# Performance work log

Measured on AMD Instinct MI355X. Metric: run time of the kernel, lower is better.

Reference implementation:

```python
import jax, jax.numpy as jnp
import numpy as np

S, H, A = 16384, 1024, 1024


def setup_inputs() -> dict:
    key = jax.random.key(0)
    k1, k2, k3, k4, k5, k6 = jax.random.split(key, 6)
    enc_out = jax.random.normal(k1, (S, 1, H), dtype=jnp.float32)
    dec_h = jax.random.normal(k2, (1, H), dtype=jnp.float32)
    mask = jax.random.randint(k3, (S, 1), 0, 2) == 1  # bool [S,1]
    # learned params (torch Linear stores weight as [out, in]; y = x @ W.T)
    W2_dec = jax.random.normal(k4, (A, H), dtype=jnp.float32) * 0.02
    W1_enc = jax.random.normal(k5, (A, H), dtype=jnp.float32) * 0.02
    V = jax.random.normal(k6, (1, A), dtype=jnp.float32) * 0.02
    return {"enc_out": enc_out, "dec_h": dec_h, "mask": mask,
            "W2_dec": W2_dec, "W1_enc": W1_enc, "V": V}


def reference(enc_out, dec_h, mask, W2_dec, W1_enc, V):
    enc = jnp.squeeze(enc_out, axis=1)            # [S, H]
    d = dec_h @ W2_dec.T                          # [1, A]
    e = enc @ W1_enc.T                            # [S, A]
    u = jnp.tanh(d + e) @ V.T                     # [S, 1]
    u = jnp.where(mask, -jnp.inf, u)              # masked logits (returned, like in-place fill)
    a = jax.nn.softmax(u, axis=0)                 # softmax over seq dim
    out = jnp.sum(a * enc, axis=0)                # [H]
    return (out, u)
```

## Files before the change

### kernel.cpp

```cpp
#include <hip/hip_runtime.h>
#include <math.h>
#include <stdint.h>

#define S_DIM 16384
#define H_DIM 1024
#define A_DIM 1024

#define MASK_NEG (-3.0e38f)

typedef __attribute__((ext_vector_type(8))) _Float16 f16x8;
typedef __attribute__((ext_vector_type(4))) float f32x4;
typedef __attribute__((address_space(3))) uint32_t as3_u32;
typedef __attribute__((address_space(1))) uint32_t as1_u32;

__device__ __forceinline__ float fast_tanh(float x) {
    float e = __expf(2.0f * x);
    return 1.0f - 2.0f * __builtin_amdgcn_rcpf(e + 1.0f);
}


__global__ __launch_bounds__(256) void prep_kernel(
        const float* __restrict__ enc, _Float16* __restrict__ enc_h,
        const float* __restrict__ W1, _Float16* __restrict__ W1_h,
        const float* __restrict__ dec_h, const float* __restrict__ W2,
        float* __restrict__ d, float* __restrict__ u_acc,
        const void* __restrict__ mask, int* __restrict__ mflag) {
    const int b = blockIdx.x;
    const int t = threadIdx.x;
    if (b < 1088) {
        const int cb = b;
        const float* src;
        _Float16* dst;
        int tb, kt;
        if (cb < 1024) { src = enc;  dst = enc_h; tb = cb >> 4; kt = cb & 15; }
        else           { src = W1;   dst = W1_h;  tb = (cb - 1024) >> 4; kt = (cb - 1024) & 15; }
        uint4* dchunk = (uint4*)dst + (size_t)(tb * 16 + kt) * 1024;
        const float* srow = src + (size_t)tb * 256 * H_DIM + kt * 32;
        #pragma unroll
        for (int it = 0; it < 4; ++it) {
            const int idx  = it * 256 + t;
            const int r    = idx >> 2;
            const int slot = idx & 3;
            const int cg   = (slot + (r >> 1)) & 3;
            const float* sp = srow + (size_t)r * H_DIM + cg * 8;
            float4 v0 = ((const float4*)sp)[0];
            float4 v1 = ((const float4*)sp)[1];
            union { _Float16 h[8]; uint4 u; } pk;
            pk.h[0] = (_Float16)v0.x; pk.h[1] = (_Float16)v0.y;
            pk.h[2] = (_Float16)v0.z; pk.h[3] = (_Float16)v0.w;
            pk.h[4] = (_Float16)v1.x; pk.h[5] = (_Float16)v1.y;
            pk.h[6] = (_Float16)v1.z; pk.h[7] = (_Float16)v1.w;
            dchunk[idx] = pk.u;
        }
        if (b < 64) u_acc[b * 256 + t] = 0.0f;
    } else if (b < 2112) {
        const int a = b - 1088;
        const float* row = W2 + (size_t)a * H_DIM;
        float s = 0.0f;
        for (int h = t; h < H_DIM; h += 256) s += dec_h[h] * row[h];
        #pragma unroll
        for (int off = 32; off; off >>= 1) s += __shfl_down(s, off, 64);
        __shared__ float wsum[4];
        if ((t & 63) == 0) wsum[t >> 6] = s;
        __syncthreads();
        if (t == 0) d[a] = wsum[0] + wsum[1] + wsum[2] + wsum[3];
    } else {
        const unsigned char* mb = (const unsigned char*)mask;
        unsigned int orv = 0;
        for (int i = t; i < S_DIM; i += 256)
            if (i & 3) orv |= mb[i];
        __shared__ int oflag;
        if (t == 0) oflag = 0;
        __syncthreads();
        if (orv) oflag = 1;
        __syncthreads();
        if (t == 0) mflag[0] = oflag;
    }
}

__global__ __launch_bounds__(512, 1) void fused_gemm_f16_2ph(
        const _Float16* __restrict__ Ag,
        const _Float16* __restrict__ Bg,
        const float* __restrict__ V,
        const float* __restrict__ d,
        float* __restrict__ u_acc) {
    __shared__ __align__(16) _Float16 AB[2][32768];

    const int tid  = threadIdx.x;
    const int wave = tid >> 6;
    const int lane = tid & 63;
    const int quad = lane >> 4;
    const int l16  = lane & 15;
    const int wm   = wave >> 2;
    const int wn   = wave & 3;
    const int s0   = blockIdx.x * 256;
    const int a0   = blockIdx.y * 256;

    const int rowoff = (wave & 3) * 64;
    const _Float16* gtile = ((wave < 4)
            ? Ag + (size_t)blockIdx.x * (16 * 8192)
            : Bg + (size_t)blockIdx.y * (16 * 8192))
          + rowoff * 32 + lane * 8;
    _Float16* lbase0 = &AB[0][((wave < 4) ? 0 : 8192) + rowoff * 32];

    const int sw = ((quad - (l16 >> 1)) & 3) * 8;
    int aoff[8], boff[4];
    #pragma unroll
    for (int mi = 0; mi < 8; ++mi)
        aoff[mi] = (wm * 128 + mi * 16 + l16) * 32 + sw;
    #pragma unroll
    for (int ni = 0; ni < 4; ++ni)
        boff[ni] = 8192 + (wn * 64 + ni * 16 + l16) * 32 + sw;

    f32x4 acc[8][4];
    #pragma unroll
    for (int mi = 0; mi < 8; ++mi)
        #pragma unroll
        for (int ni = 0; ni < 4; ++ni)
            acc[mi][ni] = (f32x4){0.f, 0.f, 0.f, 0.f};

    const _Float16* hAB = &AB[0][0];

    #pragma unroll
    for (int s = 0; s < 2; ++s)
        #pragma unroll
        for (int j = 0; j < 4; ++j)
            __builtin_amdgcn_global_load_lds(
                (const as1_u32*)(const void*)(gtile + s * 8192 + j * 512),
                (as3_u32*)(void*)(lbase0 + s * 16384 + j * 512), 16, 0, 0);

    for (int ph = 0; ph < 16; ++ph) {
        const int b = ph & 1;
        if (ph < 15) {
            #pragma unroll
            for (int s = 0; s < 2; ++s)
                #pragma unroll
                for (int j = 0; j < 4; ++j)
                    __builtin_amdgcn_global_load_lds(
                        (const as1_u32*)(const void*)(gtile + ((ph + 1) * 2 + s) * 8192 + j * 512),
                        (as3_u32*)(void*)(lbase0 + (b ^ 1) * 32768 + s * 16384 + j * 512),
                        16, 0, 0);
            asm volatile("s_waitcnt vmcnt(8)" ::: "memory");
        } else {
            asm volatile("s_waitcnt vmcnt(0)" ::: "memory");
        }
        __builtin_amdgcn_sched_barrier(0);
        __builtin_amdgcn_s_barrier();
        __builtin_amdgcn_sched_barrier(0);

        __builtin_amdgcn_s_setprio(1);
        #pragma unroll
        for (int s = 0; s < 2; ++s) {
            const int base = b * 32768 + s * 16384;
            f16x8 bf[4];
            #pragma unroll
            for (int ni = 0; ni < 4; ++ni)
                bf[ni] = *(const f16x8*)&hAB[base + boff[ni]];
            #pragma unroll
            for (int mi = 0; mi < 8; ++mi) {
                f16x8 af = *(const f16x8*)&hAB[base + aoff[mi]];
                #pragma unroll
                for (int ni = 0; ni < 4; ++ni)
                    acc[mi][ni] = __builtin_amdgcn_mfma_f32_16x16x32_f16(af, bf[ni], acc[mi][ni], 0, 0, 0);
            }
        }
        __builtin_amdgcn_s_setprio(0);
        __builtin_amdgcn_sched_barrier(0);

        if (ph < 15) {
            __builtin_amdgcn_s_barrier();
            __builtin_amdgcn_sched_barrier(0);
        }
    }

    float* P = (float*)&AB[0][0];
    float vv[4], dd[4];
    #pragma unroll
    for (int ni = 0; ni < 4; ++ni) {
        int c = a0 + wn * 64 + ni * 16 + l16;
        vv[ni] = V[c];
        dd[ni] = d[c];
    }
    #pragma unroll
    for (int mi = 0; mi < 8; ++mi) {
        #pragma unroll
        for (int reg = 0; reg < 4; ++reg) {
            float s = 0.0f;
            #pragma unroll
            for (int ni = 0; ni < 4; ++ni)
                s += vv[ni] * fast_tanh(dd[ni] + acc[mi][ni][reg]);
            #pragma unroll
            for (int off = 1; off < 16; off <<= 1)
                s += __shfl_xor(s, off, 64);
            if (l16 == 0)
                P[(wm * 128 + mi * 16 + quad * 4 + reg) * 4 + wn] = s;
        }
    }
    __syncthreads();
    if (tid < 256)
        atomicAdd(u_acc + s0 + tid,
                  P[tid * 4 + 0] + P[tid * 4 + 1] + P[tid * 4 + 2] + P[tid * 4 + 3]);
}

__global__ __launch_bounds__(512, 2) void fused_gemm_f16(
        const _Float16* __restrict__ Ag, const _Float16* __restrict__ Bg,
        const float* __restrict__ V, const float* __restrict__ d,
        float* __restrict__ u_acc) {
    __shared__ __align__(16) _Float16 AB[2][16384];

    const int tid  = threadIdx.x;
    const int wave = tid >> 6;
    const int lane = tid & 63;
    const int quad = lane >> 4;
    const int l16  = lane & 15;
    const int wm   = wave >> 2;
    const int wn   = wave & 3;
    const int s0   = blockIdx.x * 256;
    const int a0   = blockIdx.y * 256;

    const int rowoff = (wave & 3) * 64;
    const _Float16* gtile = ((wave < 4)
            ? Ag + (size_t)blockIdx.x * (16 * 8192)
            : Bg + (size_t)blockIdx.y * (16 * 8192))
          + rowoff * 32 + lane * 8;
    _Float16* lbase0 = &AB[0][((wave < 4) ? 0 : 8192) + rowoff * 32];

    const int sw = ((quad - (l16 >> 1)) & 3) * 8;
    int aoff[8], boff[4];
    #pragma unroll
    for (int mi = 0; mi < 8; ++mi)
        aoff[mi] = (wm * 128 + mi * 16 + l16) * 32 + sw;
    #pragma unroll
    for (int ni = 0; ni < 4; ++ni)
        boff[ni] = 8192 + (wn * 64 + ni * 16 + l16) * 32 + sw;

    f32x4 acc[8][4];
    #pragma unroll
    for (int mi = 0; mi < 8; ++mi)
        #pragma unroll
        for (int ni = 0; ni < 4; ++ni)
            acc[mi][ni] = (f32x4){0.f, 0.f, 0.f, 0.f};

    #pragma unroll
    for (int j = 0; j < 4; ++j)
        __builtin_amdgcn_global_load_lds(
            (const as1_u32*)(const void*)(gtile + j * 512),
            (as3_u32*)(void*)(lbase0 + j * 512), 16, 0, 0);
    __syncthreads();

    for (int kt = 0; kt < H_DIM / 32; kt += 2) {
        {
            #pragma unroll
            for (int j = 0; j < 4; ++j)
                __builtin_amdgcn_global_load_lds(
                    (const as1_u32*)(const void*)(gtile + (kt + 1) * 8192 + j * 512),
                    (as3_u32*)(void*)(lbase0 + 16384 + j * 512), 16, 0, 0);
        }
        {
            f16x8 bf[4];
            #pragma unroll
            for (int ni = 0; ni < 4; ++ni) bf[ni] = *(const f16x8*)&AB[0][boff[ni]];
            #pragma unroll
            for (int mi = 0; mi < 8; ++mi) {
                f16x8 af = *(const f16x8*)&AB[0][aoff[mi]];
                #pragma unroll
                for (int ni = 0; ni < 4; ++ni)
                    acc[mi][ni] = __builtin_amdgcn_mfma_f32_16x16x32_f16(af, bf[ni], acc[mi][ni], 0, 0, 0);
            }
        }
        __syncthreads();
        if (kt + 2 < H_DIM / 32) {
            #pragma unroll
            for (int j = 0; j < 4; ++j)
                __builtin_amdgcn_global_load_lds(
                    (const as1_u32*)(const void*)(gtile + (kt + 2) * 8192 + j * 512),
                    (as3_u32*)(void*)(lbase0 + j * 512), 16, 0, 0);
        }
        {
            f16x8 bf[4];
            #pragma unroll
            for (int ni = 0; ni < 4; ++ni) bf[ni] = *(const f16x8*)&AB[1][boff[ni]];
            #pragma unroll
            for (int mi = 0; mi < 8; ++mi) {
                f16x8 af = *(const f16x8*)&AB[1][aoff[mi]];
                #pragma unroll
                for (int ni = 0; ni < 4; ++ni)
                    acc[mi][ni] = __builtin_amdgcn_mfma_f32_16x16x32_f16(af, bf[ni], acc[mi][ni], 0, 0, 0);
            }
        }
        __syncthreads();
    }

    float* P = (float*)&AB[0][0];
    float vv[4], dd[4];
    #pragma unroll
    for (int ni = 0; ni < 4; ++ni) {
        int c = a0 + wn * 64 + ni * 16 + l16;
        vv[ni] = V[c];
        dd[ni] = d[c];
    }
    #pragma unroll
    for (int mi = 0; mi < 8; ++mi) {
        #pragma unroll
        for (int reg = 0; reg < 4; ++reg) {
            float s = 0.0f;
            #pragma unroll
            for (int ni = 0; ni < 4; ++ni)
                s += vv[ni] * fast_tanh(dd[ni] + acc[mi][ni][reg]);
            #pragma unroll
            for (int off = 1; off < 16; off <<= 1)
                s += __shfl_xor(s, off, 64);
            if (l16 == 0)
                P[(wm * 128 + mi * 16 + quad * 4 + reg) * 4 + wn] = s;
        }
    }
    __syncthreads();
    if (tid < 256)
        atomicAdd(u_acc + s0 + tid,
                  P[tid * 4 + 0] + P[tid * 4 + 1] + P[tid * 4 + 2] + P[tid * 4 + 3]);
}

__global__ __launch_bounds__(256) void fused_gemm(const float* __restrict__ enc,
                                                  const float* __restrict__ W1,
                                                  const float* __restrict__ V,
                                                  const float* __restrict__ d,
                                                  float* __restrict__ u_acc) {
    __shared__ __align__(16) float As[16][128 + 4];
    __shared__ __align__(16) float Bs[16][128 + 4];
    const int tid = threadIdx.x;
    const int tx = tid & 15, ty = tid >> 4;
    const int s0 = blockIdx.y * 128, a0 = blockIdx.x * 128;
    const int lr = tid >> 2, lc = tid & 3;
    float acc[8][8] = {};
    for (int kt = 0; kt < H_DIM / 16; ++kt) {
        const int k0 = kt * 16;
        float4 av0 = *(const float4*)(enc + (size_t)(s0 + lr)      * H_DIM + k0 + 4 * lc);
        float4 av1 = *(const float4*)(enc + (size_t)(s0 + lr + 64) * H_DIM + k0 + 4 * lc);
        float4 bv0 = *(const float4*)(W1  + (size_t)(a0 + lr)      * H_DIM + k0 + 4 * lc);
        float4 bv1 = *(const float4*)(W1  + (size_t)(a0 + lr + 64) * H_DIM + k0 + 4 * lc);
        __syncthreads();
        As[4*lc+0][lr] = av0.x; As[4*lc+1][lr] = av0.y; As[4*lc+2][lr] = av0.z; As[4*lc+3][lr] = av0.w;
        As[4*lc+0][lr+64] = av1.x; As[4*lc+1][lr+64] = av1.y; As[4*lc+2][lr+64] = av1.z; As[4*lc+3][lr+64] = av1.w;
        Bs[4*lc+0][lr] = bv0.x; Bs[4*lc+1][lr] = bv0.y; Bs[4*lc+2][lr] = bv0.z; Bs[4*lc+3][lr] = bv0.w;
        Bs[4*lc+0][lr+64] = bv1.x; Bs[4*lc+1][lr+64] = bv1.y; Bs[4*lc+2][lr+64] = bv1.z; Bs[4*lc+3][lr+64] = bv1.w;
        __syncthreads();
        #pragma unroll
        for (int k = 0; k < 16; ++k) {
            float4 A0 = *(const float4*)&As[k][8 * ty];
            float4 A1 = *(const float4*)&As[k][8 * ty + 4];
            float4 B0 = *(const float4*)&Bs[k][8 * tx];
            float4 B1 = *(const float4*)&Bs[k][8 * tx + 4];
            float ar[8] = {A0.x, A0.y, A0.z, A0.w, A1.x, A1.y, A1.z, A1.w};
            float br[8] = {B0.x, B0.y, B0.z, B0.w, B1.x, B1.y, B1.z, B1.w};
            #pragma unroll
            for (int i = 0; i < 8; ++i)
                #pragma unroll
                for (int j = 0; j < 8; ++j)
                    acc[i][j] = fmaf(ar[i], br[j], acc[i][j]);
        }
    }
    float vv[8], dd[8];
    #pragma unroll
    for (int j = 0; j < 8; ++j) { int c = a0 + 8 * tx + j; vv[j] = V[c]; dd[j] = d[c]; }
    float pu[8];
    #pragma unroll
    for (int i = 0; i < 8; ++i) {
        float s = 0.0f;
        #pragma unroll
        for (int j = 0; j < 8; ++j) s += vv[j] * fast_tanh(dd[j] + acc[i][j]);
        pu[i] = s;
    }
    __syncthreads();
    float* Pf = &As[0][0];
    #pragma unroll
    for (int i = 0; i < 8; ++i) Pf[(8 * ty + i) * 16 + tx] = pu[i];
    __syncthreads();
    if (tid < 128) {
        float s = 0.0f;
        #pragma unroll
        for (int j = 0; j < 16; ++j) s += Pf[tid * 16 + j];
        atomicAdd(u_acc + s0 + tid, s);
    }
}

__global__ __launch_bounds__(1024) void softmax_kernel(const float* __restrict__ u_acc,
                                                       const void* __restrict__ mask,
                                                       float* __restrict__ u_out,
                                                       float* __restrict__ p) {
    const int t = threadIdx.x;
    const unsigned char* mb = (const unsigned char*)mask;
    const int* mi = (const int*)mask;

    unsigned int orv = 0;
    for (int i = t; i < S_DIM; i += 1024)
        if (i & 3) orv |= mb[i];
    __shared__ int sflag;
    if (t == 0) sflag = 0;
    __syncthreads();
    if (orv) sflag = 1;
    __syncthreads();
    const int bytemask = sflag;

    float v[16];
    float lmax = -INFINITY;
    #pragma unroll
    for (int i = 0; i < 16; ++i) {
        int r = t + i * 1024;
        int m = bytemask ? (int)mb[r] : mi[r];
        float val = m ? MASK_NEG : u_acc[r];
        u_out[r] = val;
        v[i] = val;
        lmax = fmaxf(lmax, val);
    }

    __shared__ float red[16];
    __shared__ float sm, sdenom;
    #pragma unroll
    for (int off = 32; off; off >>= 1) lmax = fmaxf(lmax, __shfl_down(lmax, off, 64));
    int wid = t >> 6, lane = t & 63;
    if (lane == 0) red[wid] = lmax;
    __syncthreads();
    if (t == 0) {
        float m2 = -INFINITY;
        for (int i = 0; i < 16; ++i) m2 = fmaxf(m2, red[i]);
        sm = m2;
    }
    __syncthreads();
    const float m = sm;

    float lsum = 0.0f;
    #pragma unroll
    for (int i = 0; i < 16; ++i) {
        v[i] = expf(v[i] - m);
        lsum += v[i];
    }
    #pragma unroll
    for (int off = 32; off; off >>= 1) lsum += __shfl_down(lsum, off, 64);
    if (lane == 0) red[wid] = lsum;
    __syncthreads();
    if (t == 0) {
        float s2 = 0.0f;
        for (int i = 0; i < 16; ++i) s2 += red[i];
        sdenom = s2;
    }
    __syncthreads();
    const float inv = 1.0f / sdenom;
    #pragma unroll
    for (int i = 0; i < 16; ++i) p[t + i * 1024] = v[i] * inv;
}

__global__ __launch_bounds__(256) void tail_part(
        const _Float16* __restrict__ enc_h,
        const float* __restrict__ u_acc,
        const void* __restrict__ mask,
        const int* __restrict__ mflag,
        float* __restrict__ u_out,
        float* __restrict__ part,
        float* __restrict__ pm,
        float* __restrict__ pd) {
    const int t = threadIdx.x;
    const int b = blockIdx.x;
    const int s0 = b * 32;
    __shared__ float wsh[32];

    if (t < 32) {
        const int s = s0 + t;
        int msk = mflag[0] ? (int)((const unsigned char*)mask)[s]
                           : ((const int*)mask)[s];
        float val = msk ? MASK_NEG : u_acc[s];
        u_out[s] = val;
        float m_b = val;
        #pragma unroll
        for (int off = 16; off; off >>= 1)
            m_b = fmaxf(m_b, __shfl_xor(m_b, off, 64));
        float w = msk ? 0.0f : expf(val - m_b);
        wsh[t] = w;
        float D = w;
        #pragma unroll
        for (int off = 16; off; off >>= 1)
            D += __shfl_xor(D, off, 64);
        if (t == 0) { pm[b] = m_b; pd[b] = D; }
    }
    __syncthreads();

    const int kt    = t >> 3;
    const int cg    = (t >> 1) & 3;
    const int inner = (t & 1) * 4;
    float4 acc = {0.f, 0.f, 0.f, 0.f};
    for (int i = 0; i < 32; ++i) {
        float w = wsh[i];
        if (w != 0.0f) {
            const int s  = s0 + i;
            const int r  = s & 255;
            const int tb = s >> 8;
            const int slot = (cg - (r >> 1)) & 3;
            size_t off = ((size_t)(tb * 16 + kt) << 13) + (r << 5) + slot * 8 + inner;
            union { _Float16 h[4]; uint2 u; } e;
            e.u = *(const uint2*)(enc_h + off);
            acc.x += w * (float)e.h[0];
            acc.y += w * (float)e.h[1];
            acc.z += w * (float)e.h[2];
            acc.w += w * (float)e.h[3];
        }
    }
    ((float4*)(part + (size_t)b * 1024))[t] = acc;
}

__global__ __launch_bounds__(256) void tail_reduce(
        const float* __restrict__ part, const float* __restrict__ pm,
        const float* __restrict__ pd, float* __restrict__ out) {
    __shared__ float scale[512];
    __shared__ float red[256];
    __shared__ float ginv;
    const int t = threadIdx.x;

    red[t] = fmaxf(pm[t], pm[t + 256]);
    __syncthreads();
    #pragma unroll
    for (int off = 128; off; off >>= 1) {
        if (t < off) red[t] = fmaxf(red[t], red[t + off]);
        __syncthreads();
    }
    const float gm = red[0];
    __syncthreads();

    float sc0 = expf(pm[t] - gm);
    float sc1 = expf(pm[t + 256] - gm);
    scale[t] = sc0; scale[t + 256] = sc1;
    red[t] = sc0 * pd[t] + sc1 * pd[t + 256];
    __syncthreads();
    #pragma unroll
    for (int off = 128; off; off >>= 1) {
        if (t < off) red[t] += red[t + off];
        __syncthreads();
    }
    if (t == 0) ginv = 1.0f / red[0];
    __syncthreads();

    const int col = blockIdx.x * 16 + (t & 15);
    const int seg = t >> 4;
    float s = 0.0f;
    for (int b2 = seg * 32; b2 < seg * 32 + 32; ++b2)
        s += scale[b2] * part[(size_t)b2 * 1024 + col];
    red[t] = s;
    __syncthreads();
    if (t < 16) {
        float r = 0.0f;
        #pragma unroll
        for (int k = 0; k < 16; ++k) r += red[k * 16 + t];
        out[col] = r * ginv;
    }
}

__global__ __launch_bounds__(256) void weighted_sum(const float* __restrict__ enc,
                                                    const float* __restrict__ p,
                                                    float* __restrict__ out) {
    const int t = threadIdx.x;
    const int s0 = blockIdx.x * 32;
    const float4* encv = (const float4*)enc;
    float4 acc = {0.0f, 0.0f, 0.0f, 0.0f};
    for (int s = s0; s < s0 + 32; ++s) {
        float ps = p[s];
        float4 e = encv[(size_t)s * 256 + t];
        acc.x += ps * e.x; acc.y += ps * e.y; acc.z += ps * e.z; acc.w += ps * e.w;
    }
    atomicAdd(out + 4 * t + 0, acc.x);
    atomicAdd(out + 4 * t + 1, acc.y);
    atomicAdd(out + 4 * t + 2, acc.z);
    atomicAdd(out + 4 * t + 3, acc.w);
}
__global__ void zero_kernel(float* __restrict__ u_acc, float* __restrict__ out) {
    int i = blockIdx.x * 256 + threadIdx.x;
    if (i < S_DIM) u_acc[i] = 0.0f;
    if (i < H_DIM) out[i]   = 0.0f;
}
__global__ __launch_bounds__(256) void dec_proj(const float* __restrict__ dec_h,
                                                const float* __restrict__ W2,
                                                float* __restrict__ d) {
    int a = blockIdx.x;
    int t = threadIdx.x;
    const float* row = W2 + (size_t)a * H_DIM;
    float s = 0.0f;
    for (int h = t; h < H_DIM; h += 256) s += dec_h[h] * row[h];
    #pragma unroll
    for (int off = 32; off; off >>= 1) s += __shfl_down(s, off, 64);
    __shared__ float wsum[4];
    if ((t & 63) == 0) wsum[t >> 6] = s;
    __syncthreads();
    if (t == 0) d[a] = wsum[0] + wsum[1] + wsum[2] + wsum[3];
}

extern "C" void kernel_launch(void* const* d_in, const int* in_sizes, int n_in,
                              void* d_out, int out_size, void* d_ws, size_t ws_size,
                              hipStream_t stream) {
    const float* enc   = (const float*)d_in[0];
    const float* dec_h = (const float*)d_in[1];
    const void*  mask  = d_in[2];
    const float* W2    = (const float*)d_in[3];
    const float* W1    = (const float*)d_in[4];
    const float* V     = (const float*)d_in[5];

    float* out   = (float*)d_out;
    float* u_out = (float*)d_out + H_DIM;

    float* ws    = (float*)d_ws;
    float* d     = ws;
    float* u_acc = ws + A_DIM;
    float* p     = ws + A_DIM + S_DIM;
    float* pm    = p;
    float* pd    = p + 512;
    int*   mflag = (int*)(p + 1024);
    float* part  = ws + A_DIM + 2 * S_DIM;
    size_t f_end = (size_t)(A_DIM + 2 * S_DIM + 512 * 1024);
    _Float16* enc_h = (_Float16*)(ws + f_end);
    _Float16* W1_h  = enc_h + (size_t)S_DIM * H_DIM;
    size_t need_bytes = f_end * 4
                      + (size_t)S_DIM * H_DIM * 2
                      + (size_t)A_DIM * H_DIM * 2;

    int dev = 0;
    hipGetDevice(&dev);
    int max_lds = 0;
    hipDeviceGetAttribute(&max_lds, hipDeviceAttributeMaxSharedMemoryPerBlock, dev);

    if (ws_size >= need_bytes) {
        prep_kernel<<<2113, 256, 0, stream>>>(enc, enc_h, W1, W1_h,
                                              dec_h, W2, d, u_acc, mask, mflag);
        if (max_lds >= 131072) {
            fused_gemm_f16_2ph<<<dim3(S_DIM / 256, A_DIM / 256), 512, 0, stream>>>(
                enc_h, W1_h, V, d, u_acc);
        } else {
            fused_gemm_f16<<<dim3(S_DIM / 256, A_DIM / 256), 512, 0, stream>>>(
                enc_h, W1_h, V, d, u_acc);
        }
        tail_part<<<S_DIM / 32, 256, 0, stream>>>(enc_h, u_acc, mask, mflag,
                                                  u_out, part, pm, pd);
        tail_reduce<<<64, 256, 0, stream>>>(part, pm, pd, out);
    } else {
        zero_kernel<<<64, 256, 0, stream>>>(u_acc, out);
        dec_proj<<<A_DIM, 256, 0, stream>>>(dec_h, W2, d);
        fused_gemm<<<dim3(A_DIM / 128, S_DIM / 128), 256, 0, stream>>>(enc, W1, V, d, u_acc);
        softmax_kernel<<<1, 1024, 0, stream>>>(u_acc, mask, u_out, p);
        weighted_sum<<<S_DIM / 32, 256, 0, stream>>>(enc, p, out);
    }
}
```

Before: 168.3 us.

## Fuse fp32-to-fp16 conversion of encoder into GEMM loader, drop enc_h staging

Removes the separate pass that converts the whole encoder matrix to a swizzled fp16 copy. The GEMM's A-side waves now load fp32 rows directly, convert them in registers and store them into LDS, with loads for the next stage issued around the compute halves. The tail kernel reads fp32 encoder rows directly instead of the fp16 copy. This saves a 64MB read plus 32MB write round trip. In exchange, A tiles are re-read in fp32 by each of the 4 A-column blocks, which doubles A-side traffic, and the register-staged loads may stall MFMA more than the async LDS loads did. The fallback fp16 GEMM variant is deleted.

```diff
diff --git a/kernel.cpp b/kernel.cpp
--- a/kernel.cpp
+++ b/kernel.cpp
@@ -20,22 +20,16 @@
 
 
 __global__ __launch_bounds__(256) void prep_kernel(
-        const float* __restrict__ enc, _Float16* __restrict__ enc_h,
         const float* __restrict__ W1, _Float16* __restrict__ W1_h,
         const float* __restrict__ dec_h, const float* __restrict__ W2,
         float* __restrict__ d, float* __restrict__ u_acc,
         const void* __restrict__ mask, int* __restrict__ mflag) {
     const int b = blockIdx.x;
     const int t = threadIdx.x;
-    if (b < 1088) {
-        const int cb = b;
-        const float* src;
-        _Float16* dst;
-        int tb, kt;
-        if (cb < 1024) { src = enc;  dst = enc_h; tb = cb >> 4; kt = cb & 15; }
-        else           { src = W1;   dst = W1_h;  tb = (cb - 1024) >> 4; kt = (cb - 1024) & 15; }
-        uint4* dchunk = (uint4*)dst + (size_t)(tb * 16 + kt) * 1024;
-        const float* srow = src + (size_t)tb * 256 * H_DIM + kt * 32;
+    if (b < 64) {
+        const int tb = b >> 4, kt = b & 15;
+        uint4* dchunk = (uint4*)W1_h + (size_t)(tb * 16 + kt) * 1024;
+        const float* srow = W1 + (size_t)tb * 256 * H_DIM + kt * 32;
         #pragma unroll
         for (int it = 0; it < 4; ++it) {
             const int idx  = it * 256 + t;
@@ -52,9 +46,9 @@
             pk.h[6] = (_Float16)v1.z; pk.h[7] = (_Float16)v1.w;
             dchunk[idx] = pk.u;
         }
-        if (b < 64) u_acc[b * 256 + t] = 0.0f;
-    } else if (b < 2112) {
-        const int a = b - 1088;
+        u_acc[b * 256 + t] = 0.0f;
+    } else if (b < 1088) {
+        const int a = b - 64;
         const float* row = W2 + (size_t)a * H_DIM;
         float s = 0.0f;
         for (int h = t; h < H_DIM; h += 256) s += dec_h[h] * row[h];
@@ -79,7 +73,7 @@
 }
 
 __global__ __launch_bounds__(512, 1) void fused_gemm_f16_2ph(
-        const _Float16* __restrict__ Ag,
+        const float* __restrict__ enc,
         const _Float16* __restrict__ Bg,
         const float* __restrict__ V,
         const float* __restrict__ d,
@@ -97,11 +91,16 @@
     const int a0   = blockIdx.y * 256;
 
     const int rowoff = (wave & 3) * 64;
-    const _Float16* gtile = ((wave < 4)
-            ? Ag + (size_t)blockIdx.x * (16 * 8192)
-            : Bg + (size_t)blockIdx.y * (16 * 8192))
-          + rowoff * 32 + lane * 8;
-    _Float16* lbase0 = &AB[0][((wave < 4) ? 0 : 8192) + rowoff * 32];
+    const int lrow  = lane >> 2;
+    const int slotc = lane & 3;
+    const int cg    = (slotc + (lrow >> 1)) & 3;
+
+    const float* asrc[4];
+    #pragma unroll
+    for (int j = 0; j < 4; ++j)
+        asrc[j] = enc + (size_t)(s0 + rowoff + j * 16 + lrow) * H_DIM + cg * 8;
+    const _Float16* gtile = Bg + (size_t)blockIdx.y * (16 * 8192) + rowoff * 32 + lane * 8;
+    _Float16* lbaseB = &AB[0][8192 + rowoff * 32];
 
     const int sw = ((quad - (l16 >> 1)) & 3) * 8;
     int aoff[8], boff[4];
@@ -121,27 +120,71 @@
 
     const _Float16* hAB = &AB[0][0];
 
-    #pragma unroll
-    for (int s = 0; s < 2; ++s)
-        #pragma unroll
-        for (int j = 0; j < 4; ++j)
-            __builtin_amdgcn_global_load_lds(
-                (const as1_u32*)(const void*)(gtile + s * 8192 + j * 512),
-                (as3_u32*)(void*)(lbase0 + s * 16384 + j * 512), 16, 0, 0);
+    auto pack8 = [](float4 a, float4 b) -> uint4 {
+        union { _Float16 h[8]; uint4 u; } pk;
+        pk.h[0] = (_Float16)a.x; pk.h[1] = (_Float16)a.y;
+        pk.h[2] = (_Float16)a.z; pk.h[3] = (_Float16)a.w;
+        pk.h[4] = (_Float16)b.x; pk.h[5] = (_Float16)b.y;
+        pk.h[6] = (_Float16)b.z; pk.h[7] = (_Float16)b.w;
+        return pk.u;
+    };
+    auto COMPUTE = [&](int base) {
+        f16x8 bf[4];
+        #pragma unroll
+        for (int ni = 0; ni < 4; ++ni)
+            bf[ni] = *(const f16x8*)&hAB[base + boff[ni]];
+        #pragma unroll
+        for (int mi = 0; mi < 8; ++mi) {
+            f16x8 af = *(const f16x8*)&hAB[base + aoff[mi]];
+            #pragma unroll
+            for (int ni = 0; ni < 4; ++ni)
+                acc[mi][ni] = __builtin_amdgcn_mfma_f32_16x16x32_f16(af, bf[ni], acc[mi][ni], 0, 0, 0);
+        }
+    };
+
+    if (wave < 4) {
+        #pragma unroll
+        for (int s = 0; s < 2; ++s)
+            #pragma unroll
+            for (int j = 0; j < 4; ++j) {
+                float4 x0 = *(const float4*)(asrc[j] + s * 32);
+                float4 x1 = *(const float4*)(asrc[j] + s * 32 + 4);
+                *(uint4*)&AB[0][s * 16384 + rowoff * 32 + j * 512 + lane * 8] = pack8(x0, x1);
+            }
+        asm volatile("s_waitcnt lgkmcnt(0)" ::: "memory");
+    } else {
+        #pragma unroll
+        for (int s = 0; s < 2; ++s)
+            #pragma unroll
+            for (int j = 0; j < 4; ++j)
+                __builtin_amdgcn_global_load_lds(
+                    (const as1_u32*)(const void*)(gtile + s * 8192 + j * 512),
+                    (as3_u32*)(void*)(lbaseB + s * 16384 + j * 512), 16, 0, 0);
+    }
 
     for (int ph = 0; ph < 16; ++ph) {
         const int b = ph & 1;
+        float4 va[4][2], vb[4][2];
         if (ph < 15) {
-            #pragma unroll
-            for (int s = 0; s < 2; ++s)
+            if (wave < 4) {
+                const int kt0 = (ph + 1) * 2;
                 #pragma unroll
-                for (int j = 0; j < 4; ++j)
-                    __builtin_amdgcn_global_load_lds(
-                        (const as1_u32*)(const void*)(gtile + ((ph + 1) * 2 + s) * 8192 + j * 512),
-                        (as3_u32*)(void*)(lbase0 + (b ^ 1) * 32768 + s * 16384 + j * 512),
-                        16, 0, 0);
-            asm volatile("s_waitcnt vmcnt(8)" ::: "memory");
-        } else {
+                for (int j = 0; j < 4; ++j) {
+                    va[j][0] = *(const float4*)(asrc[j] + kt0 * 32);
+                    va[j][1] = *(const float4*)(asrc[j] + kt0 * 32 + 4);
+                }
+            } else {
+                #pragma unroll
+                for (int s = 0; s < 2; ++s)
+                    #pragma unroll
+                    for (int j = 0; j < 4; ++j)
+                        __builtin_amdgcn_global_load_lds(
+                            (const as1_u32*)(const void*)(gtile + (size_t)((ph + 1) * 2 + s) * 8192 + j * 512),
+                            (as3_u32*)(void*)(lbaseB + (b ^ 1) * 32768 + s * 16384 + j * 512),
+                            16, 0, 0);
+                asm volatile("s_waitcnt vmcnt(8)" ::: "memory");
+            }
+        } else if (wave >= 4) {
             asm volatile("s_waitcnt vmcnt(0)" ::: "memory");
         }
         __builtin_amdgcn_sched_barrier(0);
@@ -149,146 +192,39 @@
         __builtin_amdgcn_sched_barrier(0);
 
         __builtin_amdgcn_s_setprio(1);
-        #pragma unroll
-        for (int s = 0; s < 2; ++s) {
-            const int base = b * 32768 + s * 16384;
-            f16x8 bf[4];
-            #pragma unroll
-            for (int ni = 0; ni < 4; ++ni)
-                bf[ni] = *(const f16x8*)&hAB[base + boff[ni]];
-            #pragma unroll
-            for (int mi = 0; mi < 8; ++mi) {
-                f16x8 af = *(const f16x8*)&hAB[base + aoff[mi]];
-                #pragma unroll
-                for (int ni = 0; ni < 4; ++ni)
-                    acc[mi][ni] = __builtin_amdgcn_mfma_f32_16x16x32_f16(af, bf[ni], acc[mi][ni], 0, 0, 0);
-            }
-        }
+        COMPUTE(b * 32768);
         __builtin_amdgcn_s_setprio(0);
         __builtin_amdgcn_sched_barrier(0);
 
+        if (ph < 15 && wave < 4) {
+            #pragma unroll
+            for (int j = 0; j < 4; ++j)
+                *(uint4*)&AB[b ^ 1][rowoff * 32 + j * 512 + lane * 8] = pack8(va[j][0], va[j][1]);
+            const int kt1 = (ph + 1) * 2 + 1;
+            #pragma unroll
+            for (int j = 0; j < 4; ++j) {
+                vb[j][0] = *(const float4*)(asrc[j] + kt1 * 32);
+                vb[j][1] = *(const float4*)(asrc[j] + kt1 * 32 + 4);
+            }
+        }
+        __builtin_amdgcn_sched_barrier(0);
+
+        __builtin_amdgcn_s_setprio(1);
+        COMPUTE(b * 32768 + 16384);
+        __builtin_amdgcn_s_setprio(0);
+        __builtin_amdgcn_sched_barrier(0);
+
         if (ph < 15) {
+            if (wave < 4) {
+                #pragma unroll
+                for (int j = 0; j < 4; ++j)
+                    *(uint4*)&AB[b ^ 1][16384 + rowoff * 32 + j * 512 + lane * 8] = pack8(vb[j][0], vb[j][1]);
+                asm volatile("s_waitcnt lgkmcnt(0)" ::: "memory");
+            }
+            __builtin_amdgcn_sched_barrier(0);
             __builtin_amdgcn_s_barrier();
             __builtin_amdgcn_sched_barrier(0);
         }
-    }
-
-    float* P = (float*)&AB[0][0];
-    float vv[4], dd[4];
-    #pragma unroll
-    for (int ni = 0; ni < 4; ++ni) {
-        int c = a0 + wn * 64 + ni * 16 + l16;
-        vv[ni] = V[c];
-        dd[ni] = d[c];
-    }
-    #pragma unroll
-    for (int mi = 0; mi < 8; ++mi) {
-        #pragma unroll
-        for (int reg = 0; reg < 4; ++reg) {
-            float s = 0.0f;
-            #pragma unroll
-            for (int ni = 0; ni < 4; ++ni)
-                s += vv[ni] * fast_tanh(dd[ni] + acc[mi][ni][reg]);
-            #pragma unroll
-            for (int off = 1; off < 16; off <<= 1)
-                s += __shfl_xor(s, off, 64);
-            if (l16 == 0)
-                P[(wm * 128 + mi * 16 + quad * 4 + reg) * 4 + wn] = s;
-        }
-    }
-    __syncthreads();
-    if (tid < 256)
-        atomicAdd(u_acc + s0 + tid,
-                  P[tid * 4 + 0] + P[tid * 4 + 1] + P[tid * 4 + 2] + P[tid * 4 + 3]);
-}
-
-__global__ __launch_bounds__(512, 2) void fused_gemm_f16(
-        const _Float16* __restrict__ Ag, const _Float16* __restrict__ Bg,
-        const float* __restrict__ V, const float* __restrict__ d,
-        float* __restrict__ u_acc) {
-    __shared__ __align__(16) _Float16 AB[2][16384];
-
-    const int tid  = threadIdx.x;
-    const int wave = tid >> 6;
-    const int lane = tid & 63;
-    const int quad = lane >> 4;
-    const int l16  = lane & 15;
-    const int wm   = wave >> 2;
-    const int wn   = wave & 3;
-    const int s0   = blockIdx.x * 256;
-    const int a0   = blockIdx.y * 256;
-
-    const int rowoff = (wave & 3) * 64;
-    const _Float16* gtile = ((wave < 4)
-            ? Ag + (size_t)blockIdx.x * (16 * 8192)
-            : Bg + (size_t)blockIdx.y * (16 * 8192))
-          + rowoff * 32 + lane * 8;
-    _Float16* lbase0 = &AB[0][((wave < 4) ? 0 : 8192) + rowoff * 32];
-
-    const int sw = ((quad - (l16 >> 1)) & 3) * 8;
-    int aoff[8], boff[4];
-    #pragma unroll
-    for (int mi = 0; mi < 8; ++mi)
-        aoff[mi] = (wm * 128 + mi * 16 + l16) * 32 + sw;
-    #pragma unroll
-    for (int ni = 0; ni < 4; ++ni)
-        boff[ni] = 8192 + (wn * 64 + ni * 16 + l16) * 32 + sw;
-
-    f32x4 acc[8][4];
-    #pragma unroll
-    for (int mi = 0; mi < 8; ++mi)
-        #pragma unroll
-        for (int ni = 0; ni < 4; ++ni)
-            acc[mi][ni] = (f32x4){0.f, 0.f, 0.f, 0.f};
-
-    #pragma unroll
-    for (int j = 0; j < 4; ++j)
-        __builtin_amdgcn_global_load_lds(
-            (const as1_u32*)(const void*)(gtile + j * 512),
-            (as3_u32*)(void*)(lbase0 + j * 512), 16, 0, 0);
-    __syncthreads();
-
-    for (int kt = 0; kt < H_DIM / 32; kt += 2) {
-        {
-            #pragma unroll
-            for (int j = 0; j < 4; ++j)
-                __builtin_amdgcn_global_load_lds(
-                    (const as1_u32*)(const void*)(gtile + (kt + 1) * 8192 + j * 512),
-                    (as3_u32*)(void*)(lbase0 + 16384 + j * 512), 16, 0, 0);
-        }
-        {
-            f16x8 bf[4];
-            #pragma unroll
-            for (int ni = 0; ni < 4; ++ni) bf[ni] = *(const f16x8*)&AB[0][boff[ni]];
-            #pragma unroll
-            for (int mi = 0; mi < 8; ++mi) {
-                f16x8 af = *(const f16x8*)&AB[0][aoff[mi]];
-                #pragma unroll
-                for (int ni = 0; ni < 4; ++ni)
-                    acc[mi][ni] = __builtin_amdgcn_mfma_f32_16x16x32_f16(af, bf[ni], acc[mi][ni], 0, 0, 0);
-            }
-        }
-        __syncthreads();
-        if (kt + 2 < H_DIM / 32) {
-            #pragma unroll
-            for (int j = 0; j < 4; ++j)
-                __builtin_amdgcn_global_load_lds(
-                    (const as1_u32*)(const void*)(gtile + (kt + 2) * 8192 + j * 512),
-                    (as3_u32*)(void*)(lbase0 + j * 512), 16, 0, 0);
-        }
-        {
-            f16x8 bf[4];
-            #pragma unroll
-            for (int ni = 0; ni < 4; ++ni) bf[ni] = *(const f16x8*)&AB[1][boff[ni]];
-            #pragma unroll
-            for (int mi = 0; mi < 8; ++mi) {
-                f16x8 af = *(const f16x8*)&AB[1][aoff[mi]];
-                #pragma unroll
-                for (int ni = 0; ni < 4; ++ni)
-                    acc[mi][ni] = __builtin_amdgcn_mfma_f32_16x16x32_f16(af, bf[ni], acc[mi][ni], 0, 0, 0);
-            }
-        }
-        __syncthreads();
     }
 
     float* P = (float*)&AB[0][0];
@@ -450,7 +386,7 @@
 }
 
 __global__ __launch_bounds__(256) void tail_part(
-        const _Float16* __restrict__ enc_h,
+        const float* __restrict__ enc,
         const float* __restrict__ u_acc,
         const void* __restrict__ mask,
         const int* __restrict__ mflag,
@@ -483,24 +419,16 @@
     }
     __syncthreads();
 
-    const int kt    = t >> 3;
-    const int cg    = (t >> 1) & 3;
-    const int inner = (t & 1) * 4;
+    const float4* encv = (const float4*)enc;
     float4 acc = {0.f, 0.f, 0.f, 0.f};
     for (int i = 0; i < 32; ++i) {
         float w = wsh[i];
         if (w != 0.0f) {
-            const int s  = s0 + i;
-            const int r  = s & 255;
-            const int tb = s >> 8;
-            const int slot = (cg - (r >> 1)) & 3;
-            size_t off = ((size_t)(tb * 16 + kt) << 13) + (r << 5) + slot * 8 + inner;
-            union { _Float16 h[4]; uint2 u; } e;
-            e.u = *(const uint2*)(enc_h + off);
-            acc.x += w * (float)e.h[0];
-            acc.y += w * (float)e.h[1];
-            acc.z += w * (float)e.h[2];
-            acc.w += w * (float)e.h[3];
+            float4 e = encv[(size_t)(s0 + i) * 256 + t];
+            acc.x += w * e.x;
+            acc.y += w * e.y;
+            acc.z += w * e.z;
+            acc.w += w * e.w;
         }
     }
     ((float4*)(part + (size_t)b * 1024))[t] = acc;
@@ -612,28 +540,20 @@
     int*   mflag = (int*)(p + 1024);
     float* part  = ws + A_DIM + 2 * S_DIM;
     size_t f_end = (size_t)(A_DIM + 2 * S_DIM + 512 * 1024);
-    _Float16* enc_h = (_Float16*)(ws + f_end);
-    _Float16* W1_h  = enc_h + (size_t)S_DIM * H_DIM;
-    size_t need_bytes = f_end * 4
-                      + (size_t)S_DIM * H_DIM * 2
-                      + (size_t)A_DIM * H_DIM * 2;
+    _Float16* W1_h = (_Float16*)(ws + f_end);
+    size_t need_bytes = f_end * 4 + (size_t)A_DIM * H_DIM * 2;
 
     int dev = 0;
     hipGetDevice(&dev);
     int max_lds = 0;
     hipDeviceGetAttribute(&max_lds, hipDeviceAttributeMaxSharedMemoryPerBlock, dev);
 
-    if (ws_size >= need_bytes) {
-        prep_kernel<<<2113, 256, 0, stream>>>(enc, enc_h, W1, W1_h,
-                                              dec_h, W2, d, u_acc, mask, mflag);
-        if (max_lds >= 131072) {
-            fused_gemm_f16_2ph<<<dim3(S_DIM / 256, A_DIM / 256), 512, 0, stream>>>(
-                enc_h, W1_h, V, d, u_acc);
-        } else {
-            fused_gemm_f16<<<dim3(S_DIM / 256, A_DIM / 256), 512, 0, stream>>>(
-                enc_h, W1_h, V, d, u_acc);
-        }
-        tail_part<<<S_DIM / 32, 256, 0, stream>>>(enc_h, u_acc, mask, mflag,
+    if (ws_size >= need_bytes && max_lds >= 131072) {
+        prep_kernel<<<1089, 256, 0, stream>>>(W1, W1_h, dec_h, W2,
+                                              d, u_acc, mask, mflag);
+        fused_gemm_f16_2ph<<<dim3(S_DIM / 256, A_DIM / 256), 512, 0, stream>>>(
+            enc, W1_h, V, d, u_acc);
+        tail_part<<<S_DIM / 32, 256, 0, stream>>>(enc, u_acc, mask, mflag,
                                                   u_out, part, pm, pd);
         tail_reduce<<<64, 256, 0, stream>>>(part, pm, pd, out);
     } else {
```

Measured after the change: 241.8 us. +43.6%, slower.

## Fuse softmax tail into single kernel with atomics and last-block normalization

Applied to the files above, without the earlier changes.

Replaces the two-kernel tail (per-block partials plus a reduce kernel) with one kernel. Each block atomically adds its unnormalized weighted sums into the output and its exp-sum into a global denominator, and the last block to finish divides by that denominator. The per-block max subtraction is dropped and raw exp(u) is used, which relies on logits staying small enough not to overflow. This removes one launch and the partial buffer traffic, in exchange for heavy float atomic contention on 1024 output addresses.

```diff
diff --git a/kernel.cpp b/kernel.cpp
--- a/kernel.cpp
+++ b/kernel.cpp
@@ -24,7 +24,9 @@
         const float* __restrict__ W1, _Float16* __restrict__ W1_h,
         const float* __restrict__ dec_h, const float* __restrict__ W2,
         float* __restrict__ d, float* __restrict__ u_acc,
-        const void* __restrict__ mask, int* __restrict__ mflag) {
+        const void* __restrict__ mask, int* __restrict__ mflag,
+        float* __restrict__ out, float* __restrict__ Dacc,
+        int* __restrict__ cnt) {
     const int b = blockIdx.x;
     const int t = threadIdx.x;
     if (b < 1088) {
@@ -53,6 +55,8 @@
             dchunk[idx] = pk.u;
         }
         if (b < 64) u_acc[b * 256 + t] = 0.0f;
+        if (b < 4)  out[b * 256 + t]   = 0.0f;
+        if (b == 4 && t == 0) { Dacc[0] = 0.0f; cnt[0] = 0; }
     } else if (b < 2112) {
         const int a = b - 1088;
         const float* row = W2 + (size_t)a * H_DIM;
@@ -137,7 +141,7 @@
                 #pragma unroll
                 for (int j = 0; j < 4; ++j)
                     __builtin_amdgcn_global_load_lds(
-                        (const as1_u32*)(const void*)(gtile + ((ph + 1) * 2 + s) * 8192 + j * 512),
+                        (const as1_u32*)(const void*)(gtile + (size_t)((ph + 1) * 2 + s) * 8192 + j * 512),
                         (as3_u32*)(void*)(lbase0 + (b ^ 1) * 32768 + s * 16384 + j * 512),
                         16, 0, 0);
             asm volatile("s_waitcnt vmcnt(8)" ::: "memory");
@@ -318,6 +322,83 @@
     if (tid < 256)
         atomicAdd(u_acc + s0 + tid,
                   P[tid * 4 + 0] + P[tid * 4 + 1] + P[tid * 4 + 2] + P[tid * 4 + 3]);
+}
+
+__global__ __launch_bounds__(256) void tail_fused(
+        const _Float16* __restrict__ enc_h,
+        const float* __restrict__ u_acc,
+        const void* __restrict__ mask,
+        const int* __restrict__ mflag,
+        float* __restrict__ u_out,
+        float* __restrict__ out,
+        float* __restrict__ Dacc,
+        int* __restrict__ cnt) {
+    const int t = threadIdx.x;
+    const int b = blockIdx.x;
+    const int s0 = b * 32;
+    __shared__ float wsh[32];
+    __shared__ int lastf;
+    __shared__ float dsh;
+    if (t == 0) lastf = 0;
+
+    if (t < 32) {
+        const int s = s0 + t;
+        int msk = mflag[0] ? (int)((const unsigned char*)mask)[s]
+                           : ((const int*)mask)[s];
+        float val = msk ? MASK_NEG : u_acc[s];
+        u_out[s] = val;
+        float w = msk ? 0.0f : __expf(val);
+        wsh[t] = w;
+        float D = w;
+        #pragma unroll
+        for (int off = 16; off; off >>= 1)
+            D += __shfl_xor(D, off, 64);
+        if (t == 0) atomicAdd(Dacc, D);
+    }
+    __syncthreads();
+
+    const int kt    = t >> 3;
+    const int cg    = (t >> 1) & 3;
+    const int inner = (t & 1) * 4;
+    float4 acc = {0.f, 0.f, 0.f, 0.f};
+    for (int i = 0; i < 32; ++i) {
+        float w = wsh[i];
+        if (w != 0.0f) {
+            const int s  = s0 + i;
+            const int r  = s & 255;
+            const int tb = s >> 8;
+            const int slot = (cg - (r >> 1)) & 3;
+            size_t off = ((size_t)(tb * 16 + kt) << 13) + (r << 5) + slot * 8 + inner;
+            union { _Float16 h[4]; uint2 u; } e;
+            e.u = *(const uint2*)(enc_h + off);
+            acc.x += w * (float)e.h[0];
+            acc.y += w * (float)e.h[1];
+            acc.z += w * (float)e.h[2];
+            acc.w += w * (float)e.h[3];
+        }
+    }
+    atomicAdd(out + 4 * t + 0, acc.x);
+    atomicAdd(out + 4 * t + 1, acc.y);
+    atomicAdd(out + 4 * t + 2, acc.z);
+    atomicAdd(out + 4 * t + 3, acc.w);
+
+    __threadfence();
+    __syncthreads();
+    if (t == 0) {
+        int old = atomicAdd(cnt, 1);
+        if (old == 511) {
+            lastf = 1;
+            dsh = atomicAdd(Dacc, 0.0f);
+        }
+    }
+    __syncthreads();
+    if (lastf) {
+        const float inv = 1.0f / dsh;
+        for (int h = t; h < H_DIM; h += 256) {
+            float v = atomicAdd(out + h, 0.0f);
+            out[h] = v * inv;
+        }
+    }
 }
 
 __global__ __launch_bounds__(256) void fused_gemm(const float* __restrict__ enc,
@@ -449,109 +530,6 @@
     for (int i = 0; i < 16; ++i) p[t + i * 1024] = v[i] * inv;
 }
 
-__global__ __launch_bounds__(256) void tail_part(
-        const _Float16* __restrict__ enc_h,
-        const float* __restrict__ u_acc,
-        const void* __restrict__ mask,
-        const int* __restrict__ mflag,
-        float* __restrict__ u_out,
-        float* __restrict__ part,
-        float* __restrict__ pm,
-        float* __restrict__ pd) {
-    const int t = threadIdx.x;
-    const int b = blockIdx.x;
-    const int s0 = b * 32;
-    __shared__ float wsh[32];
-
-    if (t < 32) {
-        const int s = s0 + t;
-        int msk = mflag[0] ? (int)((const unsigned char*)mask)[s]
-                           : ((const int*)mask)[s];
-        float val = msk ? MASK_NEG : u_acc[s];
-        u_out[s] = val;
-        float m_b = val;
-        #pragma unroll
-        for (int off = 16; off; off >>= 1)
-            m_b = fmaxf(m_b, __shfl_xor(m_b, off, 64));
-        float w = msk ? 0.0f : expf(val - m_b);
-        wsh[t] = w;
-        float D = w;
-        #pragma unroll
-        for (int off = 16; off; off >>= 1)
-            D += __shfl_xor(D, off, 64);
-        if (t == 0) { pm[b] = m_b; pd[b] = D; }
-    }
-    __syncthreads();
-
-    const int kt    = t >> 3;
-    const int cg    = (t >> 1) & 3;
-    const int inner = (t & 1) * 4;
-    float4 acc = {0.f, 0.f, 0.f, 0.f};
-    for (int i = 0; i < 32; ++i) {
-        float w = wsh[i];
-        if (w != 0.0f) {
-            const int s  = s0 + i;
-            const int r  = s & 255;
-            const int tb = s >> 8;
-            const int slot = (cg - (r >> 1)) & 3;
-            size_t off = ((size_t)(tb * 16 + kt) << 13) + (r << 5) + slot * 8 + inner;
-            union { _Float16 h[4]; uint2 u; } e;
-            e.u = *(const uint2*)(enc_h + off);
-            acc.x += w * (float)e.h[0];
-            acc.y += w * (float)e.h[1];
-            acc.z += w * (float)e.h[2];
-            acc.w += w * (float)e.h[3];
-        }
-    }
-    ((float4*)(part + (size_t)b * 1024))[t] = acc;
-}
-
-__global__ __launch_bounds__(256) void tail_reduce(
-        const float* __restrict__ part, const float* __restrict__ pm,
-        const float* __restrict__ pd, float* __restrict__ out) {
-    __shared__ float scale[512];
-    __shared__ float red[256];
-    __shared__ float ginv;
-    const int t = threadIdx.x;
-
-    red[t] = fmaxf(pm[t], pm[t + 256]);
-    __syncthreads();
-    #pragma unroll
-    for (int off = 128; off; off >>= 1) {
-        if (t < off) red[t] = fmaxf(red[t], red[t + off]);
-        __syncthreads();
-    }
-    const float gm = red[0];
-    __syncthreads();
-
-    float sc0 = expf(pm[t] - gm);
-    float sc1 = expf(pm[t + 256] - gm);
-    scale[t] = sc0; scale[t + 256] = sc1;
-    red[t] = sc0 * pd[t] + sc1 * pd[t + 256];
-    __syncthreads();
-    #pragma unroll
-    for (int off = 128; off; off >>= 1) {
-        if (t < off) red[t] += red[t + off];
-        __syncthreads();
-    }
-    if (t == 0) ginv = 1.0f / red[0];
-    __syncthreads();
-
-    const int col = blockIdx.x * 16 + (t & 15);
-    const int seg = t >> 4;
-    float s = 0.0f;
-    for (int b2 = seg * 32; b2 < seg * 32 + 32; ++b2)
-        s += scale[b2] * part[(size_t)b2 * 1024 + col];
-    red[t] = s;
-    __syncthreads();
-    if (t < 16) {
-        float r = 0.0f;
-        #pragma unroll
-        for (int k = 0; k < 16; ++k) r += red[k * 16 + t];
-        out[col] = r * ginv;
-    }
-}
-
 __global__ __launch_bounds__(256) void weighted_sum(const float* __restrict__ enc,
                                                     const float* __restrict__ p,
                                                     float* __restrict__ out) {
@@ -607,10 +585,9 @@
     float* d     = ws;
     float* u_acc = ws + A_DIM;
     float* p     = ws + A_DIM + S_DIM;
-    float* pm    = p;
-    float* pd    = p + 512;
+    float* Dacc  = p + 512;
+    int*   cnt   = (int*)(p + 513);
     int*   mflag = (int*)(p + 1024);
-    float* part  = ws + A_DIM + 2 * S_DIM;
     size_t f_end = (size_t)(A_DIM + 2 * S_DIM + 512 * 1024);
     _Float16* enc_h = (_Float16*)(ws + f_end);
     _Float16* W1_h  = enc_h + (size_t)S_DIM * H_DIM;
@@ -625,7 +602,8 @@
 
     if (ws_size >= need_bytes) {
         prep_kernel<<<2113, 256, 0, stream>>>(enc, enc_h, W1, W1_h,
-                                              dec_h, W2, d, u_acc, mask, mflag);
+                                              dec_h, W2, d, u_acc, mask, mflag,
+                                              out, Dacc, cnt);
         if (max_lds >= 131072) {
             fused_gemm_f16_2ph<<<dim3(S_DIM / 256, A_DIM / 256), 512, 0, stream>>>(
                 enc_h, W1_h, V, d, u_acc);
@@ -633,9 +611,8 @@
             fused_gemm_f16<<<dim3(S_DIM / 256, A_DIM / 256), 512, 0, stream>>>(
                 enc_h, W1_h, V, d, u_acc);
         }
-        tail_part<<<S_DIM / 32, 256, 0, stream>>>(enc_h, u_acc, mask, mflag,
-                                                  u_out, part, pm, pd);
-        tail_reduce<<<64, 256, 0, stream>>>(part, pm, pd, out);
+        tail_fused<<<S_DIM / 32, 256, 0, stream>>>(enc_h, u_acc, mask, mflag,
+                                                   u_out, out, Dacc, cnt);
     } else {
         zero_kernel<<<64, 256, 0, stream>>>(u_acc, out);
         dec_proj<<<A_DIM, 256, 0, stream>>>(dec_h, W2, d);
```

Result: slower. 224.6 us (+33.4%).
